# Kernel optimization log

Hardware: AMD Instinct MI355X
Metric: run time of the kernel (lower is better)

The kernel has to match this reference:

```python
import jax, jax.numpy as jnp
import numpy as np

NEG_SLOPE = 0.2  # PyG GATConv default leaky_relu slope
EPS = 1e-16


def gat_conv(x, W, att_src, att_dst, bias, src, dst, heads, out_ch, concat):
    # x: [N, F_in]; W: [F_in, heads*out_ch]; att_*: [heads, out_ch]
    N = x.shape[0]
    h = (x @ W).reshape(N, heads, out_ch)                # [N, H, C]
    a_src = (h * att_src).sum(-1)                        # [N, H]
    a_dst = (h * att_dst).sum(-1)                        # [N, H]
    e = jax.nn.leaky_relu(a_src[src] + a_dst[dst], NEG_SLOPE)  # [E, H]
    # numerically stable segment softmax over incoming edges of each dst node
    e_max = jax.ops.segment_max(e, dst, num_segments=N)  # [N, H]
    e_exp = jnp.exp(e - jax.lax.stop_gradient(e_max)[dst])
    denom = jax.ops.segment_sum(e_exp, dst, num_segments=N)
    alpha = e_exp / (denom[dst] + EPS)                   # [E, H]
    msg = h[src] * alpha[:, :, None]                     # [E, H, C]
    out = jax.ops.segment_sum(msg, dst, num_segments=N)  # [N, H, C]
    if concat:
        out = out.reshape(N, heads * out_ch)
    else:
        out = out.mean(axis=1)
    return out + bias


def setup_inputs() -> dict:
    key = jax.random.key(0)
    ks = jax.random.split(key, 8)
    N, E, F_in, H, C, NC = 50000, 1600000, 256, 8, 16, 40
    x = jax.random.normal(ks[0], (N, F_in), dtype=jnp.float32)
    edge_index = jax.random.randint(ks[1], (2, E), 0, N, dtype=jnp.int64)
    s1 = 1.0 / np.sqrt(F_in)
    s2 = 1.0 / np.sqrt(H * C)
    W1 = jax.random.normal(ks[2], (F_in, H * C), dtype=jnp.float32) * s1
    att_src1 = jax.random.normal(ks[3], (H, C), dtype=jnp.float32) * 0.1
    att_dst1 = jax.random.normal(ks[4], (H, C), dtype=jnp.float32) * 0.1
    b1 = jnp.zeros((H * C,), dtype=jnp.float32)
    W2 = jax.random.normal(ks[5], (H * C, NC), dtype=jnp.float32) * s2
    att_src2 = jax.random.normal(ks[6], (1, NC), dtype=jnp.float32) * 0.1
    att_dst2 = jax.random.normal(ks[7], (1, NC), dtype=jnp.float32) * 0.1
    b2 = jnp.zeros((NC,), dtype=jnp.float32)
    return {"x": x, "edge_index": edge_index, "W1": W1, "att_src1": att_src1,
            "att_dst1": att_dst1, "b1": b1, "W2": W2, "att_src2": att_src2,
            "att_dst2": att_dst2, "b2": b2}


def reference(x, edge_index, W1, att_src1, att_dst1, b1, W2, att_src2, att_dst2, b2):
    N = x.shape[0]
    # PyG GATConv adds self-loops by default
    loops = jnp.arange(N, dtype=edge_index.dtype)
    src = jnp.concatenate([edge_index[0], loops])
    dst = jnp.concatenate([edge_index[1], loops])
    # inference mode: F.dropout is identity
    h = gat_conv(x, W1, att_src1, att_dst1, b1, src, dst, heads=8, out_ch=16, concat=True)
    h = jax.nn.elu(h)
    out = gat_conv(h, W2, att_src2, att_dst2, b2, src, dst, heads=1, out_ch=40, concat=False)
    return out
```

## Files before the change

kernel.cpp:

```cpp
#include <hip/hip_runtime.h>

#define FIN 256
#define H1 8
#define C1 16
#define D1 128
#define D2 40
#define D2P 48

#define BW_LOG 8
#define BWIDTH 256
#define B1 512

typedef float f32x4 __attribute__((ext_vector_type(4)));
typedef short bf16x8 __attribute__((ext_vector_type(8)));

static __device__ __forceinline__ float lrelu(float x){ return fmaxf(x, 0.2f*x); }
static __device__ __forceinline__ float elu(float x){ return x > 0.f ? x : __expf(x) - 1.f; }
static __device__ __forceinline__ unsigned short f2bf(float f){
  unsigned u = __float_as_uint(f);
  return (unsigned short)((u + 0x7fffu + ((u >> 16) & 1u)) >> 16);
}
static __device__ __forceinline__ float bf_lo(unsigned v){ return __uint_as_float(v << 16); }
static __device__ __forceinline__ float bf_hi(unsigned v){ return __uint_as_float(v & 0xffff0000u); }
static __device__ __forceinline__ bf16x8 pack_bf8(float4 a, float4 b){
  bf16x8 r;
  r[0]=(short)f2bf(a.x); r[1]=(short)f2bf(a.y); r[2]=(short)f2bf(a.z); r[3]=(short)f2bf(a.w);
  r[4]=(short)f2bf(b.x); r[5]=(short)f2bf(b.y); r[6]=(short)f2bf(b.z); r[7]=(short)f2bf(b.w);
  return r;
}

__global__ __launch_bounds__(256) void p1count_k(const int* __restrict__ dst, int E, int NB,
                                                 int* __restrict__ blockHist){
  extern __shared__ int hist[];
  int blk = blockIdx.x, t = threadIdx.x;
  for (int i = t; i < NB; i += 256) hist[i] = 0;
  __syncthreads();
  int CH = (E + B1 - 1) / B1;
  int lo = blk*CH, hi = min(E, lo + CH);
  for (int i = lo + t; i < hi; i += 256)
    atomicAdd(&hist[dst[i] >> BW_LOG], 1);
  __syncthreads();
  for (int b = t; b < NB; b += 256) blockHist[b*B1 + blk] = hist[b];
}

__global__ __launch_bounds__(B1) void bscan_k(const int* __restrict__ blockHist,
                                              int* __restrict__ wOff, int* __restrict__ bucketCnt){
  __shared__ int s[B1];
  int b = blockIdx.x, t = threadIdx.x;
  int v = blockHist[b*B1 + t];
  s[t] = v; __syncthreads();
  for (int o = 1; o < B1; o <<= 1){
    int u = (t >= o) ? s[t-o] : 0;
    __syncthreads();
    s[t] += u;
    __syncthreads();
  }
  wOff[b*B1 + t] = s[t] - v;
  if (t == B1-1) bucketCnt[b] = s[t];
}

__global__ __launch_bounds__(256) void p1scatter_k(const int* __restrict__ src, const int* __restrict__ dst,
                                                   int E, int NB,
                                                   const int* __restrict__ bucketCnt,
                                                   const int* __restrict__ wOff,
                                                   int* __restrict__ bucketEdges){
  extern __shared__ int curs[];
  __shared__ int sb[256];
  int blk = blockIdx.x, t = threadIdx.x;
  int v = (t < NB) ? bucketCnt[t] : 0;
  sb[t] = v; __syncthreads();
  for (int o = 1; o < 256; o <<= 1){
    int u = (t >= o) ? sb[t-o] : 0;
    __syncthreads();
    sb[t] += u;
    __syncthreads();
  }
  if (t < NB) curs[t] = (sb[t] - v) + wOff[t*B1 + blk];
  __syncthreads();
  int CH = (E + B1 - 1) / B1;
  int lo = blk*CH, hi = min(E, lo + CH);
  for (int i = lo + t; i < hi; i += 256){
    int dd = dst[i];
    int b = dd >> BW_LOG;
    int pos = atomicAdd(&curs[b], 1);
    bucketEdges[pos] = (src[i] << BW_LOG) | (dd & (BWIDTH-1));
  }
}

__global__ __launch_bounds__(BWIDTH) void p2_k(const int* __restrict__ bucketEdges,
                                               const int* __restrict__ bucketCnt, int NB,
                                               int* __restrict__ off, int* __restrict__ csr, int N){
  __shared__ int deg[BWIDTH];
  __shared__ int s[BWIDTH];
  __shared__ int cur[BWIDTH];
  __shared__ int sb[BWIDTH];
  int b = blockIdx.x, t = threadIdx.x;
  int vc = (t < NB) ? bucketCnt[t] : 0;
  sb[t] = vc; __syncthreads();
  for (int o = 1; o < BWIDTH; o <<= 1){
    int u = (t >= o) ? sb[t-o] : 0;
    __syncthreads();
    sb[t] += u;
    __syncthreads();
  }
  int e0 = (b > 0) ? sb[b-1] : 0;
  int e1 = sb[b];
  if (b == 0 && t == 0) off[N] = sb[NB-1];
  deg[t] = 0;
  __syncthreads();
  for (int i = e0 + t; i < e1; i += BWIDTH)
    atomicAdd(&deg[bucketEdges[i] & (BWIDTH-1)], 1);
  __syncthreads();
  int v = deg[t];
  s[t] = v; __syncthreads();
  for (int o = 1; o < BWIDTH; o <<= 1){
    int u = (t >= o) ? s[t-o] : 0;
    __syncthreads();
    s[t] += u;
    __syncthreads();
  }
  int excl = s[t] - v;
  int node = b*BWIDTH + t;
  if (node < N) off[node] = e0 + excl;
  cur[t] = excl;
  __syncthreads();
  for (int i = e0 + t; i < e1; i += BWIDTH){
    int pk = bucketEdges[i];
    int p = atomicAdd(&cur[pk & (BWIDTH-1)], 1);
    csr[e0 + p] = pk >> BW_LOG;
  }
}

__global__ __launch_bounds__(256) void wt_k(const float* __restrict__ W, unsigned short* __restrict__ WT){
  int n = blockIdx.x;
  int k = threadIdx.x;
  WT[n*FIN + k] = f2bf(W[(size_t)k*D1 + n]);
}

__global__ __launch_bounds__(128) void wt2_k(const float* __restrict__ W2, unsigned short* __restrict__ W2T){
  int c = blockIdx.x;
  int k = threadIdx.x;
  float v = (c < D2) ? W2[(size_t)k*D2 + c] : 0.f;
  W2T[c*D1 + k] = f2bf(v);
}

__global__ __launch_bounds__(256) void gemm1_mfma(const float* __restrict__ x,
    const unsigned short* __restrict__ W1T,
    const float* __restrict__ attS, const float* __restrict__ attD,
    unsigned short* __restrict__ h1b, float* __restrict__ aS, float* __restrict__ aD, int N){
  int tid = threadIdx.x;
  int w = tid >> 6, lane = tid & 63;
  int lr = lane & 15, lg = lane >> 4;
  int wm = w >> 1, wn = w & 1;
  int m0 = blockIdx.x * 64;

  int rowA[2];
  #pragma unroll
  for (int mi=0;mi<2;mi++){
    int r = m0 + wm*32 + mi*16 + lr;
    rowA[mi] = (r < N) ? r : (N-1);
  }

  f32x4 acc[2][4];
  #pragma unroll
  for (int mi=0;mi<2;mi++)
    #pragma unroll
    for (int ni=0;ni<4;ni++) acc[mi][ni] = (f32x4){0.f,0.f,0.f,0.f};

  #pragma unroll
  for (int ks = 0; ks < 8; ++ks){
    int k0 = ks*32 + lg*8;
    bf16x8 a[2], b[4];
    #pragma unroll
    for (int mi=0;mi<2;mi++){
      const float* px = x + (size_t)rowA[mi]*FIN + k0;
      float4 v0 = *(const float4*)px;
      float4 v1 = *(const float4*)(px+4);
      a[mi] = pack_bf8(v0, v1);
    }
    #pragma unroll
    for (int ni=0;ni<4;ni++){
      int col = wn*64 + ni*16 + lr;
      b[ni] = *(const bf16x8*)(W1T + (size_t)col*FIN + k0);
    }
    #pragma unroll
    for (int mi=0;mi<2;mi++)
      #pragma unroll
      for (int ni=0;ni<4;ni++)
        acc[mi][ni] = __builtin_amdgcn_mfma_f32_16x16x32_bf16(a[mi], b[ni], acc[mi][ni], 0, 0, 0);
  }

  #pragma unroll
  for (int mi=0;mi<2;mi++){
    #pragma unroll
    for (int ni=0;ni<4;ni++){
      int h = wn*4 + ni;
      int col = wn*64 + ni*16 + lr;
      float sS = attS[h*C1 + lr], sD = attD[h*C1 + lr];
      #pragma unroll
      for (int i=0;i<4;i++){
        int row = m0 + wm*32 + mi*16 + 4*lg + i;
        float v = acc[mi][ni][i];
        float pS = v*sS, pD = v*sD;
        pS += __shfl_xor(pS, 1); pD += __shfl_xor(pD, 1);
        pS += __shfl_xor(pS, 2); pD += __shfl_xor(pD, 2);
        pS += __shfl_xor(pS, 4); pD += __shfl_xor(pD, 4);
        pS += __shfl_xor(pS, 8); pD += __shfl_xor(pD, 8);
        if (row < N){
          h1b[(size_t)row*D1 + col] = f2bf(v);
          if (lr == 0){ aS[row*H1 + h] = pS; aD[row*H1 + h] = pD; }
        }
      }
    }
  }
}

__global__ __launch_bounds__(256) void gemm2_mfma(const unsigned short* __restrict__ x2b,
    const unsigned short* __restrict__ W2T,
    const float* __restrict__ attS2, const float* __restrict__ attD2,
    unsigned short* __restrict__ h2b, float* __restrict__ aS2, float* __restrict__ aD2, int N){
  int tid = threadIdx.x;
  int w = tid >> 6, lane = tid & 63;
  int lr = lane & 15, lg = lane >> 4;
  int m0 = blockIdx.x*128 + w*32;

  int rowA[2];
  #pragma unroll
  for (int mi=0;mi<2;mi++){
    int r = m0 + mi*16 + lr;
    rowA[mi] = (r < N) ? r : (N-1);
  }

  f32x4 acc[2][3];
  #pragma unroll
  for (int mi=0;mi<2;mi++)
    #pragma unroll
    for (int ni=0;ni<3;ni++) acc[mi][ni] = (f32x4){0.f,0.f,0.f,0.f};

  #pragma unroll
  for (int ks = 0; ks < 4; ++ks){
    int k0 = ks*32 + lg*8;
    bf16x8 a[2], b[3];
    #pragma unroll
    for (int mi=0;mi<2;mi++)
      a[mi] = *(const bf16x8*)(x2b + (size_t)rowA[mi]*D1 + k0);
    #pragma unroll
    for (int ni=0;ni<3;ni++){
      int col = ni*16 + lr;
      b[ni] = *(const bf16x8*)(W2T + (size_t)col*D1 + k0);
    }
    #pragma unroll
    for (int mi=0;mi<2;mi++)
      #pragma unroll
      for (int ni=0;ni<3;ni++)
        acc[mi][ni] = __builtin_amdgcn_mfma_f32_16x16x32_bf16(a[mi], b[ni], acc[mi][ni], 0, 0, 0);
  }

  float attSv[3], attDv[3];
  #pragma unroll
  for (int ni=0;ni<3;ni++){
    int col = ni*16 + lr;
    attSv[ni] = (col < D2) ? attS2[col] : 0.f;
    attDv[ni] = (col < D2) ? attD2[col] : 0.f;
  }
  #pragma unroll
  for (int mi=0;mi<2;mi++){
    #pragma unroll
    for (int i=0;i<4;i++){
      int row = m0 + mi*16 + 4*lg + i;
      float pS = 0.f, pD = 0.f;
      #pragma unroll
      for (int ni=0;ni<3;ni++){
        pS += acc[mi][ni][i]*attSv[ni];
        pD += acc[mi][ni][i]*attDv[ni];
      }
      pS += __shfl_xor(pS, 1); pD += __shfl_xor(pD, 1);
      pS += __shfl_xor(pS, 2); pD += __shfl_xor(pD, 2);
      pS += __shfl_xor(pS, 4); pD += __shfl_xor(pD, 4);
      pS += __shfl_xor(pS, 8); pD += __shfl_xor(pD, 8);
      if (row < N){
        #pragma unroll
        for (int ni=0;ni<3;ni++){
          int col = ni*16 + lr;
          if (col < D2) h2b[(size_t)row*D2 + col] = f2bf(acc[mi][ni][i]);
        }
        if (lr == 0){ aS2[row] = pS; aD2[row] = pD; }
      }
    }
  }
}

__global__ __launch_bounds__(64) void node1_k(const unsigned short* __restrict__ h1b,
    const float* __restrict__ aS, const float* __restrict__ aD,
    const int* __restrict__ off, const int* __restrict__ csr,
    const float* __restrict__ b1, unsigned short* __restrict__ x2b, int N){
  int n = blockIdx.x;
  int lane = threadIdx.x;
  int c = lane*2;
  int h = lane >> 3;
  float ad = aD[n*H1+h];
  float p = __expf(lrelu(aS[n*H1+h] + ad));
  float d = p;
  unsigned hv = *(const unsigned*)&h1b[(size_t)n*D1 + c];
  float acc0 = p*bf_lo(hv), acc1 = p*bf_hi(hv);
  int i = off[n], e = off[n+1];
  for (; i < e && (i & 3); ++i){
    int s = csr[i];
    float pp = __expf(lrelu(aS[s*H1+h] + ad));
    unsigned vv = *(const unsigned*)&h1b[(size_t)s*D1 + c];
    d += pp; acc0 += pp*bf_lo(vv); acc1 += pp*bf_hi(vv);
  }
  for (; i+8 <= e; i += 8){
    int4 ca = *(const int4*)&csr[i];
    int4 cb = *(const int4*)&csr[i+4];
    int s[8] = {ca.x,ca.y,ca.z,ca.w,cb.x,cb.y,cb.z,cb.w};
    float a[8]; unsigned v[8];
    #pragma unroll
    for (int u=0;u<8;u++) a[u] = aS[s[u]*H1+h];
    #pragma unroll
    for (int u=0;u<8;u++) v[u] = *(const unsigned*)&h1b[(size_t)s[u]*D1 + c];
    #pragma unroll
    for (int u=0;u<8;u++){
      float pp = __expf(lrelu(a[u]+ad));
      d += pp; acc0 += pp*bf_lo(v[u]); acc1 += pp*bf_hi(v[u]);
    }
  }
  for (; i < e; ++i){
    int s = csr[i];
    float pp = __expf(lrelu(aS[s*H1+h] + ad));
    unsigned vv = *(const unsigned*)&h1b[(size_t)s*D1 + c];
    d += pp; acc0 += pp*bf_lo(vv); acc1 += pp*bf_hi(vv);
  }
  float inv = 1.f/d;
  float o0 = elu(acc0*inv + b1[c]);
  float o1 = elu(acc1*inv + b1[c+1]);
  unsigned pk = (unsigned)f2bf(o0) | ((unsigned)f2bf(o1) << 16);
  *(unsigned*)&x2b[(size_t)n*D1 + c] = pk;
}

__global__ __launch_bounds__(64) void node2_k(const unsigned short* __restrict__ h2b,
    const float* __restrict__ aS2, const float* __restrict__ aD2,
    const int* __restrict__ off, const int* __restrict__ csr,
    const float* __restrict__ b2, float* __restrict__ out, int N){
  int n = blockIdx.x;
  int lane = threadIdx.x;
  bool act = lane < 20;
  int c = lane*2;
  float ad = aD2[n];
  float ps = __expf(lrelu(aS2[n] + ad));
  float d = ps;
  float acc0 = 0.f, acc1 = 0.f;
  if (act){
    unsigned v = *(const unsigned*)&h2b[(size_t)n*D2 + c];
    acc0 = ps*bf_lo(v); acc1 = ps*bf_hi(v);
  }
  int i = off[n], e = off[n+1];
  for (; i < e && (i & 3); ++i){
    int s = csr[i];
    float pp = __expf(lrelu(aS2[s] + ad));
    d += pp;
    if (act){
      unsigned vv = *(const unsigned*)&h2b[(size_t)s*D2 + c];
      acc0 += pp*bf_lo(vv); acc1 += pp*bf_hi(vv);
    }
  }
  for (; i+8 <= e; i += 8){
    int4 ca = *(const int4*)&csr[i];
    int4 cb = *(const int4*)&csr[i+4];
    int s[8] = {ca.x,ca.y,ca.z,ca.w,cb.x,cb.y,cb.z,cb.w};
    float a[8]; unsigned v[8];
    #pragma unroll
    for (int u=0;u<8;u++) a[u] = aS2[s[u]];
    if (act){
      #pragma unroll
      for (int u=0;u<8;u++) v[u] = *(const unsigned*)&h2b[(size_t)s[u]*D2 + c];
    } else {
      #pragma unroll
      for (int u=0;u<8;u++) v[u] = 0u;
    }
    #pragma unroll
    for (int u=0;u<8;u++){
      float pp = __expf(lrelu(a[u]+ad));
      d += pp; acc0 += pp*bf_lo(v[u]); acc1 += pp*bf_hi(v[u]);
    }
  }
  for (; i < e; ++i){
    int s = csr[i];
    float pp = __expf(lrelu(aS2[s] + ad));
    d += pp;
    if (act){
      unsigned vv = *(const unsigned*)&h2b[(size_t)s*D2 + c];
      acc0 += pp*bf_lo(vv); acc1 += pp*bf_hi(vv);
    }
  }
  if (act){
    float inv = 1.f/d;
    out[(size_t)n*D2 + c]     = acc0*inv + b2[c];
    out[(size_t)n*D2 + c + 1] = acc1*inv + b2[c+1];
  }
}

extern "C" void kernel_launch(void* const* d_in, const int* in_sizes, int n_in,
                              void* d_out, int out_size, void* d_ws, size_t ws_size,
                              hipStream_t stream){
  const float* x     = (const float*)d_in[0];
  const int*   ei    = (const int*)d_in[1];
  const float* W1    = (const float*)d_in[2];
  const float* attS1 = (const float*)d_in[3];
  const float* attD1 = (const float*)d_in[4];
  const float* b1    = (const float*)d_in[5];
  const float* W2    = (const float*)d_in[6];
  const float* attS2 = (const float*)d_in[7];
  const float* attD2 = (const float*)d_in[8];
  const float* b2    = (const float*)d_in[9];
  float* out = (float*)d_out;

  int N = in_sizes[0] / FIN;
  int E = in_sizes[1] / 2;
  const int* src = ei;
  const int* dst = ei + E;
  int NB = (N + BWIDTH - 1) >> BW_LOG;

  char* ws = (char*)d_ws;
  size_t o = 0;
  auto alloc = [&](size_t bytes) -> void* {
    void* p = ws + o;
    o += (bytes + 255) & ~size_t(255);
    return p;
  };
  unsigned short* h1b = (unsigned short*)alloc((size_t)N*D1*sizeof(unsigned short));
  unsigned short* x2b = (unsigned short*)alloc((size_t)N*D1*sizeof(unsigned short));
  unsigned short* h2b = (unsigned short*)alloc((size_t)N*D2*sizeof(unsigned short));
  float* aS1   = (float*)alloc((size_t)N*H1*sizeof(float));
  float* aD1   = (float*)alloc((size_t)N*H1*sizeof(float));
  float* aS2   = (float*)alloc((size_t)N*sizeof(float));
  float* aD2   = (float*)alloc((size_t)N*sizeof(float));
  int*   off   = (int*)alloc((size_t)(N+1)*sizeof(int));
  int*   csr   = (int*)alloc((size_t)E*sizeof(int));
  int*   blockHist   = (int*)alloc((size_t)NB*B1*sizeof(int));
  int*   wOff        = (int*)alloc((size_t)NB*B1*sizeof(int));
  int*   bucketCnt   = (int*)alloc((size_t)NB*sizeof(int));
  int*   bucketEdges = (int*)alloc((size_t)E*sizeof(int));
  unsigned short* W1T = (unsigned short*)alloc((size_t)D1*FIN*sizeof(unsigned short));
  unsigned short* W2T = (unsigned short*)alloc((size_t)D2P*D1*sizeof(unsigned short));

  size_t smNB = (size_t)NB*sizeof(int);
  p1count_k<<<B1, 256, smNB, stream>>>(dst, E, NB, blockHist);
  bscan_k<<<NB, B1, 0, stream>>>(blockHist, wOff, bucketCnt);
  p1scatter_k<<<B1, 256, smNB, stream>>>(src, dst, E, NB, bucketCnt, wOff, bucketEdges);
  p2_k<<<NB, BWIDTH, 0, stream>>>(bucketEdges, bucketCnt, NB, off, csr, N);
  wt_k<<<D1, 256, 0, stream>>>(W1, W1T);
  wt2_k<<<D2P, 128, 0, stream>>>(W2, W2T);
  gemm1_mfma<<<(N+63)/64, 256, 0, stream>>>(x, W1T, attS1, attD1, h1b, aS1, aD1, N);
  node1_k<<<N, 64, 0, stream>>>(h1b, aS1, aD1, off, csr, b1, x2b, N);
  gemm2_mfma<<<(N+127)/128, 256, 0, stream>>>(x2b, W2T, attS2, attD2, h2b, aS2, aD2, N);
  node2_k<<<N, 64, 0, stream>>>(h2b, aS2, aD2, off, csr, b2, out, N);
}
```

Measured before the change: 223.1 us.

## Split edge loop across wave sub-groups with wider bf16 loads in node kernels

```diff
diff --git a/kernel.cpp b/kernel.cpp
--- a/kernel.cpp
+++ b/kernel.cpp
@@ -9,7 +9,7 @@
 
 #define BW_LOG 8
 #define BWIDTH 256
-#define B1 512
+#define B1 128
 
 typedef float f32x4 __attribute__((ext_vector_type(4)));
 typedef short bf16x8 __attribute__((ext_vector_type(8)));
@@ -296,46 +296,57 @@
     const float* __restrict__ b1, unsigned short* __restrict__ x2b, int N){
   int n = blockIdx.x;
   int lane = threadIdx.x;
-  int c = lane*2;
-  int h = lane >> 3;
+  int half = lane >> 5, l32 = lane & 31;
+  int c = l32*4;
+  int h = l32 >> 2;
   float ad = aD[n*H1+h];
-  float p = __expf(lrelu(aS[n*H1+h] + ad));
-  float d = p;
-  unsigned hv = *(const unsigned*)&h1b[(size_t)n*D1 + c];
-  float acc0 = p*bf_lo(hv), acc1 = p*bf_hi(hv);
-  int i = off[n], e = off[n+1];
-  for (; i < e && (i & 3); ++i){
+  float d = 0.f, a0 = 0.f, a1 = 0.f, a2 = 0.f, a3 = 0.f;
+  if (half == 0){
+    float p = __expf(lrelu(aS[n*H1+h] + ad));
+    uint2 hv = *(const uint2*)&h1b[(size_t)n*D1 + c];
+    d = p;
+    a0 = p*bf_lo(hv.x); a1 = p*bf_hi(hv.x);
+    a2 = p*bf_lo(hv.y); a3 = p*bf_hi(hv.y);
+  }
+  int e = off[n+1];
+  int i = off[n] + half;
+  for (; i + 6 < e; i += 8){
+    int s0=csr[i], s1=csr[i+2], s2=csr[i+4], s3=csr[i+6];
+    float e0=aS[s0*H1+h], e1=aS[s1*H1+h], e2=aS[s2*H1+h], e3=aS[s3*H1+h];
+    uint2 v0 = *(const uint2*)&h1b[(size_t)s0*D1+c];
+    uint2 v1 = *(const uint2*)&h1b[(size_t)s1*D1+c];
+    uint2 v2 = *(const uint2*)&h1b[(size_t)s2*D1+c];
+    uint2 v3 = *(const uint2*)&h1b[(size_t)s3*D1+c];
+    float p0=__expf(lrelu(e0+ad)), p1=__expf(lrelu(e1+ad));
+    float p2=__expf(lrelu(e2+ad)), p3=__expf(lrelu(e3+ad));
+    d += p0+p1+p2+p3;
+    a0 += p0*bf_lo(v0.x)+p1*bf_lo(v1.x)+p2*bf_lo(v2.x)+p3*bf_lo(v3.x);
+    a1 += p0*bf_hi(v0.x)+p1*bf_hi(v1.x)+p2*bf_hi(v2.x)+p3*bf_hi(v3.x);
+    a2 += p0*bf_lo(v0.y)+p1*bf_lo(v1.y)+p2*bf_lo(v2.y)+p3*bf_lo(v3.y);
+    a3 += p0*bf_hi(v0.y)+p1*bf_hi(v1.y)+p2*bf_hi(v2.y)+p3*bf_hi(v3.y);
+  }
+  for (; i < e; i += 2){
     int s = csr[i];
     float pp = __expf(lrelu(aS[s*H1+h] + ad));
-    unsigned vv = *(const unsigned*)&h1b[(size_t)s*D1 + c];
-    d += pp; acc0 += pp*bf_lo(vv); acc1 += pp*bf_hi(vv);
-  }
-  for (; i+8 <= e; i += 8){
-    int4 ca = *(const int4*)&csr[i];
-    int4 cb = *(const int4*)&csr[i+4];
-    int s[8] = {ca.x,ca.y,ca.z,ca.w,cb.x,cb.y,cb.z,cb.w};
-    float a[8]; unsigned v[8];
-    #pragma unroll
-    for (int u=0;u<8;u++) a[u] = aS[s[u]*H1+h];
-    #pragma unroll
-    for (int u=0;u<8;u++) v[u] = *(const unsigned*)&h1b[(size_t)s[u]*D1 + c];
-    #pragma unroll
-    for (int u=0;u<8;u++){
-      float pp = __expf(lrelu(a[u]+ad));
-      d += pp; acc0 += pp*bf_lo(v[u]); acc1 += pp*bf_hi(v[u]);
-    }
-  }
-  for (; i < e; ++i){
-    int s = csr[i];
-    float pp = __expf(lrelu(aS[s*H1+h] + ad));
-    unsigned vv = *(const unsigned*)&h1b[(size_t)s*D1 + c];
-    d += pp; acc0 += pp*bf_lo(vv); acc1 += pp*bf_hi(vv);
-  }
-  float inv = 1.f/d;
-  float o0 = elu(acc0*inv + b1[c]);
-  float o1 = elu(acc1*inv + b1[c+1]);
-  unsigned pk = (unsigned)f2bf(o0) | ((unsigned)f2bf(o1) << 16);
-  *(unsigned*)&x2b[(size_t)n*D1 + c] = pk;
+    uint2 vv = *(const uint2*)&h1b[(size_t)s*D1 + c];
+    d += pp;
+    a0 += pp*bf_lo(vv.x); a1 += pp*bf_hi(vv.x);
+    a2 += pp*bf_lo(vv.y); a3 += pp*bf_hi(vv.y);
+  }
+  d  += __shfl_xor(d, 32);
+  a0 += __shfl_xor(a0, 32); a1 += __shfl_xor(a1, 32);
+  a2 += __shfl_xor(a2, 32); a3 += __shfl_xor(a3, 32);
+  if (half == 0){
+    float inv = 1.f/d;
+    float o0 = elu(a0*inv + b1[c]);
+    float o1 = elu(a1*inv + b1[c+1]);
+    float o2 = elu(a2*inv + b1[c+2]);
+    float o3 = elu(a3*inv + b1[c+3]);
+    uint2 pk;
+    pk.x = (unsigned)f2bf(o0) | ((unsigned)f2bf(o1) << 16);
+    pk.y = (unsigned)f2bf(o2) | ((unsigned)f2bf(o3) << 16);
+    *(uint2*)&x2b[(size_t)n*D1 + c] = pk;
+  }
 }
 
 __global__ __launch_bounds__(64) void node2_k(const unsigned short* __restrict__ h2b,
@@ -344,59 +355,63 @@
     const float* __restrict__ b2, float* __restrict__ out, int N){
   int n = blockIdx.x;
   int lane = threadIdx.x;
-  bool act = lane < 20;
-  int c = lane*2;
+  int g = lane >> 4, l16 = lane & 15;
+  int c = l16*4;
+  bool act = l16 < 10;
   float ad = aD2[n];
-  float ps = __expf(lrelu(aS2[n] + ad));
-  float d = ps;
-  float acc0 = 0.f, acc1 = 0.f;
-  if (act){
-    unsigned v = *(const unsigned*)&h2b[(size_t)n*D2 + c];
-    acc0 = ps*bf_lo(v); acc1 = ps*bf_hi(v);
-  }
-  int i = off[n], e = off[n+1];
-  for (; i < e && (i & 3); ++i){
+  float d = 0.f, a0 = 0.f, a1 = 0.f, a2 = 0.f, a3 = 0.f;
+  if (g == 0){
+    float p = __expf(lrelu(aS2[n] + ad));
+    d = p;
+    if (act){
+      uint2 v = *(const uint2*)&h2b[(size_t)n*D2 + c];
+      a0 = p*bf_lo(v.x); a1 = p*bf_hi(v.x);
+      a2 = p*bf_lo(v.y); a3 = p*bf_hi(v.y);
+    }
+  }
+  int e = off[n+1];
+  int i = off[n] + g;
+  for (; i + 12 < e; i += 16){
+    int s0=csr[i], s1=csr[i+4], s2=csr[i+8], s3=csr[i+12];
+    float e0=aS2[s0], e1=aS2[s1], e2=aS2[s2], e3=aS2[s3];
+    uint2 v0, v1, v2, v3;
+    if (act){
+      v0 = *(const uint2*)&h2b[(size_t)s0*D2+c];
+      v1 = *(const uint2*)&h2b[(size_t)s1*D2+c];
+      v2 = *(const uint2*)&h2b[(size_t)s2*D2+c];
+      v3 = *(const uint2*)&h2b[(size_t)s3*D2+c];
+    } else { v0=v1=v2=v3=make_uint2(0u,0u); }
+    float p0=__expf(lrelu(e0+ad)), p1=__expf(lrelu(e1+ad));
+    float p2=__expf(lrelu(e2+ad)), p3=__expf(lrelu(e3+ad));
+    d += p0+p1+p2+p3;
+    a0 += p0*bf_lo(v0.x)+p1*bf_lo(v1.x)+p2*bf_lo(v2.x)+p3*bf_lo(v3.x);
+    a1 += p0*bf_hi(v0.x)+p1*bf_hi(v1.x)+p2*bf_hi(v2.x)+p3*bf_hi(v3.x);
+    a2 += p0*bf_lo(v0.y)+p1*bf_lo(v1.y)+p2*bf_lo(v2.y)+p3*bf_lo(v3.y);
+    a3 += p0*bf_hi(v0.y)+p1*bf_hi(v1.y)+p2*bf_hi(v2.y)+p3*bf_hi(v3.y);
+  }
+  for (; i < e; i += 4){
     int s = csr[i];
     float pp = __expf(lrelu(aS2[s] + ad));
     d += pp;
     if (act){
-      unsigned vv = *(const unsigned*)&h2b[(size_t)s*D2 + c];
-      acc0 += pp*bf_lo(vv); acc1 += pp*bf_hi(vv);
-    }
-  }
-  for (; i+8 <= e; i += 8){
-    int4 ca = *(const int4*)&csr[i];
-    int4 cb = *(const int4*)&csr[i+4];
-    int s[8] = {ca.x,ca.y,ca.z,ca.w,cb.x,cb.y,cb.z,cb.w};
-    float a[8]; unsigned v[8];
-    #pragma unroll
-    for (int u=0;u<8;u++) a[u] = aS2[s[u]];
-    if (act){
-      #pragma unroll
-      for (int u=0;u<8;u++) v[u] = *(const unsigned*)&h2b[(size_t)s[u]*D2 + c];
-    } else {
-      #pragma unroll
-      for (int u=0;u<8;u++) v[u] = 0u;
-    }
-    #pragma unroll
-    for (int u=0;u<8;u++){
-      float pp = __expf(lrelu(a[u]+ad));
-      d += pp; acc0 += pp*bf_lo(v[u]); acc1 += pp*bf_hi(v[u]);
-    }
-  }
-  for (; i < e; ++i){
-    int s = csr[i];
-    float pp = __expf(lrelu(aS2[s] + ad));
-    d += pp;
-    if (act){
-      unsigned vv = *(const unsigned*)&h2b[(size_t)s*D2 + c];
-      acc0 += pp*bf_lo(vv); acc1 += pp*bf_hi(vv);
-    }
-  }
-  if (act){
+      uint2 vv = *(const uint2*)&h2b[(size_t)s*D2 + c];
+      a0 += pp*bf_lo(vv.x); a1 += pp*bf_hi(vv.x);
+      a2 += pp*bf_lo(vv.y); a3 += pp*bf_hi(vv.y);
+    }
+  }
+  d  += __shfl_xor(d, 16);  d  += __shfl_xor(d, 32);
+  a0 += __shfl_xor(a0, 16); a0 += __shfl_xor(a0, 32);
+  a1 += __shfl_xor(a1, 16); a1 += __shfl_xor(a1, 32);
+  a2 += __shfl_xor(a2, 16); a2 += __shfl_xor(a2, 32);
+  a3 += __shfl_xor(a3, 16); a3 += __shfl_xor(a3, 32);
+  if (g == 0 && act){
     float inv = 1.f/d;
-    out[(size_t)n*D2 + c]     = acc0*inv + b2[c];
-    out[(size_t)n*D2 + c + 1] = acc1*inv + b2[c+1];
+    float4 o;
+    o.x = a0*inv + b2[c];
+    o.y = a1*inv + b2[c+1];
+    o.z = a2*inv + b2[c+2];
+    o.w = a3*inv + b2[c+3];
+    *(float4*)&out[(size_t)n*D2 + c] = o;
   }
 }
 
```

After: 230.7 us. 3.4% more time.

## Merge independent kernels via block-range dispatch to cut launches and overlap work

Applied to the files above, without the earlier changes.

```diff
diff --git a/kernel.cpp b/kernel.cpp
--- a/kernel.cpp
+++ b/kernel.cpp
@@ -29,18 +29,30 @@
   return r;
 }
 
-__global__ __launch_bounds__(256) void p1count_k(const int* __restrict__ dst, int E, int NB,
-                                                 int* __restrict__ blockHist){
-  extern __shared__ int hist[];
-  int blk = blockIdx.x, t = threadIdx.x;
-  for (int i = t; i < NB; i += 256) hist[i] = 0;
-  __syncthreads();
-  int CH = (E + B1 - 1) / B1;
-  int lo = blk*CH, hi = min(E, lo + CH);
-  for (int i = lo + t; i < hi; i += 256)
-    atomicAdd(&hist[dst[i] >> BW_LOG], 1);
-  __syncthreads();
-  for (int b = t; b < NB; b += 256) blockHist[b*B1 + blk] = hist[b];
+__global__ __launch_bounds__(256) void f1_k(const int* __restrict__ dst, int E, int NB,
+                                            int* __restrict__ blockHist,
+                                            const float* __restrict__ W1, unsigned short* __restrict__ W1T,
+                                            const float* __restrict__ W2, unsigned short* __restrict__ W2T){
+  int b = blockIdx.x, t = threadIdx.x;
+  if (b < B1){
+    __shared__ int hist[256];
+    hist[t] = 0;
+    __syncthreads();
+    int CH = (E + B1 - 1) / B1;
+    int lo = b*CH, hi = min(E, lo + CH);
+    for (int i = lo + t; i < hi; i += 256)
+      atomicAdd(&hist[dst[i] >> BW_LOG], 1);
+    __syncthreads();
+    for (int i = t; i < NB; i += 256) blockHist[i*B1 + b] = hist[i];
+  } else if (b < B1 + 128){
+    int n = b - B1;
+    W1T[n*FIN + t] = f2bf(W1[(size_t)t*D1 + n]);
+  } else {
+    int c = (b - B1 - 128)*2 + (t >> 7);
+    int k = t & 127;
+    float v = (c < D2) ? W2[(size_t)k*D2 + c] : 0.f;
+    W2T[c*D1 + k] = f2bf(v);
+  }
 }
 
 __global__ __launch_bounds__(B1) void bscan_k(const int* __restrict__ blockHist,
@@ -59,96 +71,37 @@
   if (t == B1-1) bucketCnt[b] = s[t];
 }
 
-__global__ __launch_bounds__(256) void p1scatter_k(const int* __restrict__ src, const int* __restrict__ dst,
-                                                   int E, int NB,
-                                                   const int* __restrict__ bucketCnt,
-                                                   const int* __restrict__ wOff,
-                                                   int* __restrict__ bucketEdges){
-  extern __shared__ int curs[];
-  __shared__ int sb[256];
-  int blk = blockIdx.x, t = threadIdx.x;
-  int v = (t < NB) ? bucketCnt[t] : 0;
-  sb[t] = v; __syncthreads();
-  for (int o = 1; o < 256; o <<= 1){
-    int u = (t >= o) ? sb[t-o] : 0;
-    __syncthreads();
-    sb[t] += u;
-    __syncthreads();
-  }
-  if (t < NB) curs[t] = (sb[t] - v) + wOff[t*B1 + blk];
-  __syncthreads();
-  int CH = (E + B1 - 1) / B1;
-  int lo = blk*CH, hi = min(E, lo + CH);
-  for (int i = lo + t; i < hi; i += 256){
-    int dd = dst[i];
-    int b = dd >> BW_LOG;
-    int pos = atomicAdd(&curs[b], 1);
-    bucketEdges[pos] = (src[i] << BW_LOG) | (dd & (BWIDTH-1));
-  }
-}
-
-__global__ __launch_bounds__(BWIDTH) void p2_k(const int* __restrict__ bucketEdges,
-                                               const int* __restrict__ bucketCnt, int NB,
-                                               int* __restrict__ off, int* __restrict__ csr, int N){
-  __shared__ int deg[BWIDTH];
-  __shared__ int s[BWIDTH];
-  __shared__ int cur[BWIDTH];
-  __shared__ int sb[BWIDTH];
-  int b = blockIdx.x, t = threadIdx.x;
-  int vc = (t < NB) ? bucketCnt[t] : 0;
-  sb[t] = vc; __syncthreads();
-  for (int o = 1; o < BWIDTH; o <<= 1){
-    int u = (t >= o) ? sb[t-o] : 0;
-    __syncthreads();
-    sb[t] += u;
-    __syncthreads();
-  }
-  int e0 = (b > 0) ? sb[b-1] : 0;
-  int e1 = sb[b];
-  if (b == 0 && t == 0) off[N] = sb[NB-1];
-  deg[t] = 0;
-  __syncthreads();
-  for (int i = e0 + t; i < e1; i += BWIDTH)
-    atomicAdd(&deg[bucketEdges[i] & (BWIDTH-1)], 1);
-  __syncthreads();
-  int v = deg[t];
-  s[t] = v; __syncthreads();
-  for (int o = 1; o < BWIDTH; o <<= 1){
-    int u = (t >= o) ? s[t-o] : 0;
-    __syncthreads();
-    s[t] += u;
-    __syncthreads();
-  }
-  int excl = s[t] - v;
-  int node = b*BWIDTH + t;
-  if (node < N) off[node] = e0 + excl;
-  cur[t] = excl;
-  __syncthreads();
-  for (int i = e0 + t; i < e1; i += BWIDTH){
-    int pk = bucketEdges[i];
-    int p = atomicAdd(&cur[pk & (BWIDTH-1)], 1);
-    csr[e0 + p] = pk >> BW_LOG;
-  }
-}
-
-__global__ __launch_bounds__(256) void wt_k(const float* __restrict__ W, unsigned short* __restrict__ WT){
-  int n = blockIdx.x;
-  int k = threadIdx.x;
-  WT[n*FIN + k] = f2bf(W[(size_t)k*D1 + n]);
-}
-
-__global__ __launch_bounds__(128) void wt2_k(const float* __restrict__ W2, unsigned short* __restrict__ W2T){
-  int c = blockIdx.x;
-  int k = threadIdx.x;
-  float v = (c < D2) ? W2[(size_t)k*D2 + c] : 0.f;
-  W2T[c*D1 + k] = f2bf(v);
-}
-
-__global__ __launch_bounds__(256) void gemm1_mfma(const float* __restrict__ x,
-    const unsigned short* __restrict__ W1T,
+__global__ __launch_bounds__(256) void f3_k(
+    const float* __restrict__ x, const unsigned short* __restrict__ W1T,
     const float* __restrict__ attS, const float* __restrict__ attD,
-    unsigned short* __restrict__ h1b, float* __restrict__ aS, float* __restrict__ aD, int N){
+    unsigned short* __restrict__ h1b, float* __restrict__ aS, float* __restrict__ aD, int N, int G1,
+    const int* __restrict__ src, const int* __restrict__ dst, int E, int NB,
+    const int* __restrict__ bucketCnt, const int* __restrict__ wOff, int* __restrict__ bucketEdges){
   int tid = threadIdx.x;
+  if ((int)blockIdx.x >= G1){
+    __shared__ int curs[256];
+    __shared__ int sb[256];
+    int blk = blockIdx.x - G1;
+    int v = (tid < NB) ? bucketCnt[tid] : 0;
+    sb[tid] = v; __syncthreads();
+    for (int o = 1; o < 256; o <<= 1){
+      int u = (tid >= o) ? sb[tid-o] : 0;
+      __syncthreads();
+      sb[tid] += u;
+      __syncthreads();
+    }
+    if (tid < NB) curs[tid] = (sb[tid] - v) + wOff[tid*B1 + blk];
+    __syncthreads();
+    int CH = (E + B1 - 1) / B1;
+    int lo = blk*CH, hi = min(E, lo + CH);
+    for (int i = lo + tid; i < hi; i += 256){
+      int dd = dst[i];
+      int b = dd >> BW_LOG;
+      int pos = atomicAdd(&curs[b], 1);
+      bucketEdges[pos] = (src[i] << BW_LOG) | (dd & (BWIDTH-1));
+    }
+    return;
+  }
   int w = tid >> 6, lane = tid & 63;
   int lr = lane & 15, lg = lane >> 4;
   int wm = w >> 1, wn = w & 1;
@@ -212,6 +165,50 @@
         }
       }
     }
+  }
+}
+
+__global__ __launch_bounds__(BWIDTH) void p2_k(const int* __restrict__ bucketEdges,
+                                               const int* __restrict__ bucketCnt, int NB,
+                                               int* __restrict__ off, int* __restrict__ csr, int N){
+  __shared__ int deg[BWIDTH];
+  __shared__ int s[BWIDTH];
+  __shared__ int cur[BWIDTH];
+  __shared__ int sb[BWIDTH];
+  int b = blockIdx.x, t = threadIdx.x;
+  int vc = (t < NB) ? bucketCnt[t] : 0;
+  sb[t] = vc; __syncthreads();
+  for (int o = 1; o < BWIDTH; o <<= 1){
+    int u = (t >= o) ? sb[t-o] : 0;
+    __syncthreads();
+    sb[t] += u;
+    __syncthreads();
+  }
+  int e0 = (b > 0) ? sb[b-1] : 0;
+  int e1 = sb[b];
+  if (b == 0 && t == 0) off[N] = sb[NB-1];
+  deg[t] = 0;
+  __syncthreads();
+  for (int i = e0 + t; i < e1; i += BWIDTH)
+    atomicAdd(&deg[bucketEdges[i] & (BWIDTH-1)], 1);
+  __syncthreads();
+  int v = deg[t];
+  s[t] = v; __syncthreads();
+  for (int o = 1; o < BWIDTH; o <<= 1){
+    int u = (t >= o) ? s[t-o] : 0;
+    __syncthreads();
+    s[t] += u;
+    __syncthreads();
+  }
+  int excl = s[t] - v;
+  int node = b*BWIDTH + t;
+  if (node < N) off[node] = e0 + excl;
+  cur[t] = excl;
+  __syncthreads();
+  for (int i = e0 + t; i < e1; i += BWIDTH){
+    int pk = bucketEdges[i];
+    int p = atomicAdd(&cur[pk & (BWIDTH-1)], 1);
+    csr[e0 + p] = pk >> BW_LOG;
   }
 }
 
@@ -444,14 +441,13 @@
   unsigned short* W1T = (unsigned short*)alloc((size_t)D1*FIN*sizeof(unsigned short));
   unsigned short* W2T = (unsigned short*)alloc((size_t)D2P*D1*sizeof(unsigned short));
 
-  size_t smNB = (size_t)NB*sizeof(int);
-  p1count_k<<<B1, 256, smNB, stream>>>(dst, E, NB, blockHist);
+  int G1 = (N + 63) / 64;
+
+  f1_k<<<B1 + 128 + 24, 256, 0, stream>>>(dst, E, NB, blockHist, W1, W1T, W2, W2T);
   bscan_k<<<NB, B1, 0, stream>>>(blockHist, wOff, bucketCnt);
-  p1scatter_k<<<B1, 256, smNB, stream>>>(src, dst, E, NB, bucketCnt, wOff, bucketEdges);
+  f3_k<<<G1 + B1, 256, 0, stream>>>(x, W1T, attS1, attD1, h1b, aS1, aD1, N, G1,
+                                    src, dst, E, NB, bucketCnt, wOff, bucketEdges);
   p2_k<<<NB, BWIDTH, 0, stream>>>(bucketEdges, bucketCnt, NB, off, csr, N);
-  wt_k<<<D1, 256, 0, stream>>>(W1, W1T);
-  wt2_k<<<D2P, 128, 0, stream>>>(W2, W2T);
-  gemm1_mfma<<<(N+63)/64, 256, 0, stream>>>(x, W1T, attS1, attD1, h1b, aS1, aD1, N);
   node1_k<<<N, 64, 0, stream>>>(h1b, aS1, aD1, off, csr, b1, x2b, N);
   gemm2_mfma<<<(N+127)/128, 256, 0, stream>>>(x2b, W2T, attS2, attD2, h2b, aS2, aD2, N);
   node2_k<<<N, 64, 0, stream>>>(h2b, aS2, aD2, off, csr, b2, out, N);
```

New measurement: 206.0 us. 7.6% less time.
